# Performance work log

Measured on AMD Instinct MI355X. Metric: run time of the kernel, lower is better.

## Reference

```python
import jax, jax.numpy as jnp
import numpy as np

N_NODES = 100000
N_EDGES = 1600000
D = 128
N_GRAPHS = 8


def setup_inputs() -> dict:
    key = jax.random.key(0)
    ks = jax.random.split(key, 10)
    x = jax.random.normal(ks[0], (N_NODES, D), dtype=jnp.float32)
    src = jax.random.randint(ks[1], (N_EDGES,), 0, N_NODES)
    dst = jax.random.randint(ks[2], (N_EDGES,), 0, N_NODES)
    graph_ids = jnp.sort(jax.random.randint(ks[3], (N_NODES,), 0, N_GRAPHS))
    s = 1.0 / np.sqrt(D)
    W1 = jax.random.normal(ks[4], (D, D), dtype=jnp.float32) * s
    b1 = jnp.zeros((D,), dtype=jnp.float32)
    W2 = jax.random.normal(ks[5], (D, D), dtype=jnp.float32) * s
    b2 = jnp.zeros((D,), dtype=jnp.float32)
    prelu_a = jnp.full((1,), 0.25, dtype=jnp.float32)
    lin_W = jax.random.normal(ks[6], (D, 1), dtype=jnp.float32) * s
    lin_b = jnp.zeros((1,), dtype=jnp.float32)
    return {"x": x, "src": src, "dst": dst, "graph_ids": graph_ids,
            "W1": W1, "b1": b1, "W2": W2, "b2": b2,
            "prelu_a": prelu_a, "lin_W": lin_W, "lin_b": lin_b}


def _gcn_layer(h, src, dst, n_src, n_dst, W, b):
    # GraphConv with symmetric ('both') normalization: D^{-1/2} A D^{-1/2} H W + b
    h = h @ W                                      # [N, D] small GEMM
    m = h[src] * n_src[:, None]                    # [E, D] gather (irregular)
    agg = jax.ops.segment_sum(m, dst, num_segments=N_NODES)  # scatter-add
    return agg * n_dst[:, None] + b


def reference(x, src, dst, graph_ids, W1, b1, W2, b2, prelu_a, lin_W, lin_b):
    ones_e = jnp.ones((src.shape[0],), dtype=x.dtype)
    deg_out = jnp.maximum(jax.ops.segment_sum(ones_e, src, num_segments=N_NODES), 1.0)
    deg_in = jnp.maximum(jax.ops.segment_sum(ones_e, dst, num_segments=N_NODES), 1.0)
    n_src = jax.lax.rsqrt(deg_out)[src]            # per-edge source norm
    n_dst = jax.lax.rsqrt(deg_in)                  # per-node dest norm

    h = _gcn_layer(x, src, dst, n_src, n_dst, W1, b1)
    h = jax.nn.relu(h)
    h = _gcn_layer(h, src, dst, n_src, n_dst, W2, b2)
    h = jax.nn.relu(h)

    # dgl.mean_nodes: per-graph mean over nodes
    sums = jax.ops.segment_sum(h, graph_ids, num_segments=N_GRAPHS)   # [G, D]
    cnt = jax.ops.segment_sum(jnp.ones((N_NODES,), h.dtype), graph_ids,
                              num_segments=N_GRAPHS)
    pooled = sums / jnp.maximum(cnt, 1.0)[:, None]

    # PReLU (single shared slope) -> Linear -> Sigmoid
    pooled = jnp.where(pooled > 0, pooled, prelu_a[0] * pooled)
    out = jax.nn.sigmoid(pooled @ lin_W + lin_b)   # [G, 1]
    return out
```

## Files before the change

kernel.cpp:

```cpp
#include <hip/hip_runtime.h>
#include <hip/hip_bf16.h>

#define NN 100000
#define NE 1600000
#define DD 128
#define NG 8

#define BSH 8
#define KB 391
#define BMASK 255
#define PB 512
#define CHUNK 3125
#define SCAN_N (KB * PB)
#define GHB 98

typedef unsigned short u16;
typedef unsigned char u8;
typedef __attribute__((ext_vector_type(8))) short short8;
typedef __attribute__((ext_vector_type(4))) float f32x4;
typedef __attribute__((ext_vector_type(2))) float f32x2;

static __device__ __forceinline__ u16 f2bf(float f) {
  unsigned u = __float_as_uint(f);
  u += 0x7fffu + ((u >> 16) & 1);
  return (u16)(u >> 16);
}
static __device__ __forceinline__ u8 f2fp8(float f) {
  return (u8)(__builtin_amdgcn_cvt_pk_fp8_f32(f, f, 0, false) & 0xFF);
}

__global__ void conv_xscale(const float* __restrict__ in, const float* __restrict__ rs_out,
                            u8* __restrict__ out, int n8) {
  int i = blockIdx.x * blockDim.x + threadIdx.x;
  if (i >= n8) return;
  float w = rs_out[i >> 4];
  const float4* p = (const float4*)(in + (size_t)i * 8);
  float4 a = p[0], b = p[1];
  int lo = 0, hi = 0;
  lo = __builtin_amdgcn_cvt_pk_fp8_f32(a.x * w, a.y * w, lo, false);
  lo = __builtin_amdgcn_cvt_pk_fp8_f32(a.z * w, a.w * w, lo, true);
  hi = __builtin_amdgcn_cvt_pk_fp8_f32(b.x * w, b.y * w, hi, false);
  hi = __builtin_amdgcn_cvt_pk_fp8_f32(b.z * w, b.w * w, hi, true);
  ((uint2*)out)[i] = make_uint2((unsigned)lo, (unsigned)hi);
}

__global__ __launch_bounds__(256) void p1x(const int* __restrict__ src,
                                           const int* __restrict__ dst,
                                           int* __restrict__ countsS,
                                           int* __restrict__ countsD,
                                           const float* __restrict__ W1,
                                           const float* __restrict__ W2,
                                           u16* __restrict__ Wt1,
                                           u16* __restrict__ Wt2,
                                           const int* __restrict__ gid,
                                           int* __restrict__ cnt_part,
                                           float* __restrict__ pooled) {
  __shared__ int hs[KB], hd[KB];
  __shared__ int h8[NG];
  int t = threadIdx.x, b = blockIdx.x;
  if (b < PB) {
    for (int i = t; i < KB; i += 256) { hs[i] = 0; hd[i] = 0; }
    __syncthreads();
    int e0 = b * CHUNK;
    for (int i = t; i < CHUNK; i += 256) {
      atomicAdd(&hs[src[e0 + i] >> BSH], 1);
      atomicAdd(&hd[dst[e0 + i] >> BSH], 1);
    }
    __syncthreads();
    for (int i = t; i < KB; i += 256) {
      countsS[i * PB + b] = hs[i];
      countsD[i * PB + b] = hd[i];
    }
  } else if (b < PB + 128) {
    int i = (b - PB) * 256 + t;
    if (i < DD * DD) {
      int n = i >> 7, k = i & 127;
      Wt1[i] = f2bf(W1[k * DD + n]);
    } else {
      int i2 = i - DD * DD;
      int n = i2 >> 7, k = i2 & 127;
      Wt2[i2] = f2bf(W2[k * DD + n]);
    }
  } else if (b < PB + 128 + GHB) {
    int blk = b - PB - 128;
    if (t < NG) h8[t] = 0;
    __syncthreads();
    for (int i = blk * 256 + t; i < NN; i += GHB * 256)
      atomicAdd(&h8[gid[i]], 1);
    __syncthreads();
    if (t < NG) cnt_part[blk * NG + t] = h8[t];
  } else {
    for (int i = t; i < NG * DD; i += 256) pooled[i] = 0.f;
  }
}

__global__ __launch_bounds__(256) void scanA(int* __restrict__ countsS,
                                             int* __restrict__ countsD,
                                             int* __restrict__ totS,
                                             int* __restrict__ totD) {
  __shared__ int data[PB];
  __shared__ int part[256];
  int b = blockIdx.x;
  int isS = (b < KB);
  int k = isS ? b : b - KB;
  int* counts = isS ? countsS : countsD;
  int* tot = isS ? totS : totD;
  int t = threadIdx.x;
  int* c = counts + (size_t)k * PB;
  data[t] = c[t];
  data[t + 256] = c[t + 256];
  __syncthreads();
  int a0 = data[2 * t], a1 = data[2 * t + 1];
  int s = a0 + a1;
  part[t] = s;
  __syncthreads();
  for (int off = 1; off < 256; off <<= 1) {
    int v = (t >= off) ? part[t - off] : 0;
    __syncthreads();
    part[t] += v;
    __syncthreads();
  }
  int ex = part[t] - s;
  data[2 * t] = ex;
  data[2 * t + 1] = ex + a0;
  __syncthreads();
  c[t] = data[t];
  c[t + 256] = data[t + 256];
  if (t == 255) tot[k] = part[255];
}

__global__ __launch_bounds__(256) void scanB(const int* __restrict__ totS,
                                             const int* __restrict__ totD,
                                             int* __restrict__ baseS,
                                             int* __restrict__ baseD) {
  __shared__ int data[512];
  __shared__ int part[256];
  const int* tot = blockIdx.x ? totD : totS;
  int* base = blockIdx.x ? baseD : baseS;
  int t = threadIdx.x;
  data[t] = (t < KB) ? tot[t] : 0;
  data[t + 256] = (t + 256 < KB) ? tot[t + 256] : 0;
  __syncthreads();
  int a0 = data[2 * t], a1 = data[2 * t + 1];
  int s = a0 + a1;
  part[t] = s;
  __syncthreads();
  for (int off = 1; off < 256; off <<= 1) {
    int v = (t >= off) ? part[t - off] : 0;
    __syncthreads();
    part[t] += v;
    __syncthreads();
  }
  int ex = part[t] - s;
  int i0 = 2 * t, i1 = 2 * t + 1;
  if (i0 <= KB) base[i0] = ex;
  if (i1 <= KB) base[i1] = ex + a0;
}

__global__ __launch_bounds__(256) void p2_both(const int* __restrict__ src,
                                               const int* __restrict__ dst,
                                               const int* __restrict__ countsS,
                                               const int* __restrict__ countsD,
                                               const int* __restrict__ baseS,
                                               const int* __restrict__ baseD,
                                               u8* __restrict__ recsS,
                                               unsigned* __restrict__ recsD) {
  __shared__ int curS[KB], curD[KB];
  int t = threadIdx.x, blk = blockIdx.x;
  for (int i = t; i < KB; i += 256) {
    curS[i] = countsS[i * PB + blk] + baseS[i];
    curD[i] = countsD[i * PB + blk] + baseD[i];
  }
  __syncthreads();
  int e0 = blk * CHUNK;
  for (int i = t; i < CHUNK; i += 256) {
    int s = src[e0 + i];
    int d = dst[e0 + i];
    int ps = atomicAdd(&curS[s >> BSH], 1);
    recsS[ps] = (u8)(s & BMASK);
    int pd = atomicAdd(&curD[d >> BSH], 1);
    recsD[pd] = (unsigned)s | ((unsigned)(d & BMASK) << 17);
  }
}

__global__ __launch_bounds__(256) void sd_p3(const u8* __restrict__ recsS,
                                             const int* __restrict__ baseS,
                                             float* __restrict__ rs_out,
                                             const unsigned* __restrict__ recsD,
                                             const int* __restrict__ baseD,
                                             int* __restrict__ csr_src,
                                             int* __restrict__ cursor_end,
                                             int* __restrict__ deg_in,
                                             float* __restrict__ rs_in) {
  __shared__ int hist[256];
  __shared__ int part[256];
  int t = threadIdx.x;
  if (blockIdx.x < KB) {
    int k = blockIdx.x;
    int rbeg = baseS[k];
    int rend = baseS[k + 1];
    hist[t] = 0;
    __syncthreads();
    for (int i = rbeg + t; i < rend; i += 256) atomicAdd(&hist[recsS[i]], 1);
    __syncthreads();
    int n = (k << BSH) + t;
    if (n < NN) rs_out[n] = rsqrtf(fmaxf((float)hist[t], 1.f));
  } else {
    int k = blockIdx.x - KB;
    int rbeg = baseD[k];
    int rend = baseD[k + 1];
    hist[t] = 0;
    __syncthreads();
    for (int i = rbeg + t; i < rend; i += 256) atomicAdd(&hist[recsD[i] >> 17], 1);
    __syncthreads();
    int h = hist[t];
    part[t] = h;
    __syncthreads();
    for (int off = 1; off < 256; off <<= 1) {
      int v = (t >= off) ? part[t - off] : 0;
      __syncthreads();
      part[t] += v;
      __syncthreads();
    }
    int run = rbeg + part[t] - h;
    int n = (k << BSH) + t;
    if (n < NN) {
      cursor_end[n] = run + h;
      deg_in[n] = h;
      rs_in[n] = rsqrtf(fmaxf((float)h, 1.f));
    }
    hist[t] = run;
    __syncthreads();
    for (int i = rbeg + t; i < rend; i += 256) {
      unsigned r = recsD[i];
      int pos = atomicAdd(&hist[r >> 17], 1);
      csr_src[pos] = (int)(r & 0x1FFFF);
    }
  }
}

__global__ __launch_bounds__(256) void gather_agg_fp8(
    const uint4* __restrict__ Hv, const int* __restrict__ csr_src,
    const int* __restrict__ cursor_end, const int* __restrict__ deg_in,
    u16* __restrict__ agg) {
  int node = blockIdx.x * 32 + (threadIdx.x >> 3);
  if (node >= NN) return;
  int q = threadIdx.x & 7;
  int end = cursor_end[node];
  int j = end - deg_in[node];
  float acc[16];
#pragma unroll
  for (int i = 0; i < 16; ++i) acc[i] = 0.f;
#define ACCV(v) { f32x2 t_;                                                        \
  t_ = __builtin_amdgcn_cvt_pk_f32_fp8((int)(v).x, false); acc[0] += t_.x;  acc[1] += t_.y;  \
  t_ = __builtin_amdgcn_cvt_pk_f32_fp8((int)(v).x, true);  acc[2] += t_.x;  acc[3] += t_.y;  \
  t_ = __builtin_amdgcn_cvt_pk_f32_fp8((int)(v).y, false); acc[4] += t_.x;  acc[5] += t_.y;  \
  t_ = __builtin_amdgcn_cvt_pk_f32_fp8((int)(v).y, true);  acc[6] += t_.x;  acc[7] += t_.y;  \
  t_ = __builtin_amdgcn_cvt_pk_f32_fp8((int)(v).z, false); acc[8] += t_.x;  acc[9] += t_.y;  \
  t_ = __builtin_amdgcn_cvt_pk_f32_fp8((int)(v).z, true);  acc[10] += t_.x; acc[11] += t_.y; \
  t_ = __builtin_amdgcn_cvt_pk_f32_fp8((int)(v).w, false); acc[12] += t_.x; acc[13] += t_.y; \
  t_ = __builtin_amdgcn_cvt_pk_f32_fp8((int)(v).w, true);  acc[14] += t_.x; acc[15] += t_.y; }
  for (; j + 4 <= end; j += 4) {
    int s0 = csr_src[j + 0];
    int s1 = csr_src[j + 1];
    int s2 = csr_src[j + 2];
    int s3 = csr_src[j + 3];
    uint4 v0 = Hv[(size_t)s0 * 8 + q];
    uint4 v1 = Hv[(size_t)s1 * 8 + q];
    uint4 v2 = Hv[(size_t)s2 * 8 + q];
    uint4 v3 = Hv[(size_t)s3 * 8 + q];
    ACCV(v0) ACCV(v1) ACCV(v2) ACCV(v3)
  }
  for (; j < end; ++j) {
    uint4 v = Hv[(size_t)csr_src[j] * 8 + q];
    ACCV(v)
  }
#undef ACCV
  uint4 o0, o1;
  o0.x = (unsigned)f2bf(acc[0])  | ((unsigned)f2bf(acc[1])  << 16);
  o0.y = (unsigned)f2bf(acc[2])  | ((unsigned)f2bf(acc[3])  << 16);
  o0.z = (unsigned)f2bf(acc[4])  | ((unsigned)f2bf(acc[5])  << 16);
  o0.w = (unsigned)f2bf(acc[6])  | ((unsigned)f2bf(acc[7])  << 16);
  o1.x = (unsigned)f2bf(acc[8])  | ((unsigned)f2bf(acc[9])  << 16);
  o1.y = (unsigned)f2bf(acc[10]) | ((unsigned)f2bf(acc[11]) << 16);
  o1.z = (unsigned)f2bf(acc[12]) | ((unsigned)f2bf(acc[13]) << 16);
  o1.w = (unsigned)f2bf(acc[14]) | ((unsigned)f2bf(acc[15]) << 16);
  u16* op = agg + (size_t)node * DD + q * 16;
  *(uint4*)op = o0;
  *(uint4*)(op + 8) = o1;
}

#define GEMM_PRE                                                              \
  __shared__ uint4 Wl4[2048];                                      \
  int tid = threadIdx.x;                                                      \
  {                                                                           \
    const uint4* Wg4 = (const uint4*)Wt;                                      \
    for (int i = tid; i < 2048; i += 256) {                                   \
      int row = i >> 4, c = i & 15;                                           \
      Wl4[(row << 4) | (c ^ (row & 15))] = Wg4[i];                            \
    }                                                                         \
  }                                                                           \
  int wid = tid >> 6;                                                         \
  int lane = tid & 63;                                                        \
  int l15 = lane & 15;                                                        \
  int kg = lane >> 4;                                                         \
  int rowbase = blockIdx.x * 128 + wid * 32;                                  \
  f32x4 acc[2][8];                                                            \
  short8 a[2][4];                                                             \
  _Pragma("unroll")                                                           \
  for (int t = 0; t < 2; ++t) {                                               \
    int arow = rowbase + t * 16 + l15;                                        \
    bool ok = arow < NN;                                                      \
    const u16* aptr = Ab + (size_t)arow * DD + kg * 8;                        \
    _Pragma("unroll")                                                         \
    for (int kt = 0; kt < 4; ++kt) {                                          \
      a[t][kt] = ok ? *(const short8*)(aptr + kt * 32)                        \
                    : (short8){0, 0, 0, 0, 0, 0, 0, 0};                       \
      acc[0][kt] = (f32x4){0.f, 0.f, 0.f, 0.f};                               \
      acc[0][kt + 4] = (f32x4){0.f, 0.f, 0.f, 0.f};                           \
      acc[1][kt] = (f32x4){0.f, 0.f, 0.f, 0.f};                               \
      acc[1][kt + 4] = (f32x4){0.f, 0.f, 0.f, 0.f};                           \
    }                                                                         \
  }                                                                           \
  __syncthreads();                                                            \
  _Pragma("unroll")                                                           \
  for (int n = 0; n < 8; ++n) {                                               \
    _Pragma("unroll")                                                         \
    for (int kt = 0; kt < 4; ++kt) {                                          \
      short8 b = *(const short8*)(Wl4 + (((n * 16 + l15) << 4) |              \
                                         ((kg + kt * 4) ^ l15)));             \
      acc[0][n] = __builtin_amdgcn_mfma_f32_16x16x32_bf16(a[0][kt], b, acc[0][n], 0, 0, 0); \
      acc[1][n] = __builtin_amdgcn_mfma_f32_16x16x32_bf16(a[1][kt], b, acc[1][n], 0, 0, 0); \
    }                                                                         \
  }

__global__ __launch_bounds__(256) void gemm_mfma_fp8out(
    const u16* __restrict__ Ab, const u16* __restrict__ Wt,
    const float* __restrict__ bias, const float* __restrict__ rs,
    const float* __restrict__ post, u8* __restrict__ Cb) {
  GEMM_PRE
#pragma unroll
  for (int t = 0; t < 2; ++t) {
    int crow0 = rowbase + t * 16 + kg * 4;
#pragma unroll
    for (int j = 0; j < 4; ++j) {
      int r = crow0 + j;
      if (r < NN) {
        float s = rs[r];
        float ps = post[r];
#pragma unroll
        for (int n = 0; n < 8; ++n) {
          float v = fmaxf(acc[t][n][j] * s + bias[n * 16 + l15], 0.f) * ps;
          Cb[(size_t)r * DD + n * 16 + l15] = f2fp8(v);
        }
      }
    }
  }
}

__global__ __launch_bounds__(256) void gemm_mfma_pool(
    const u16* __restrict__ Ab, const u16* __restrict__ Wt,
    const float* __restrict__ bias, const float* __restrict__ rs,
    const int* __restrict__ gid, float* __restrict__ pooled) {
  __shared__ float pl[NG * DD];
  for (int i = threadIdx.x; i < NG * DD; i += 256) pl[i] = 0.f;
  GEMM_PRE
  float pacc[8];
#pragma unroll
  for (int n = 0; n < 8; ++n) pacc[n] = 0.f;
  int curg = -1;
#pragma unroll
  for (int t = 0; t < 2; ++t) {
    int crow0 = rowbase + t * 16 + kg * 4;
#pragma unroll
    for (int j = 0; j < 4; ++j) {
      int r = crow0 + j;
      if (r < NN) {
        int g = gid[r];
        if (g != curg) {
          if (curg >= 0) {
#pragma unroll
            for (int n = 0; n < 8; ++n) {
              atomicAdd(&pl[curg * DD + n * 16 + l15], pacc[n]);
              pacc[n] = 0.f;
            }
          }
          curg = g;
        }
        float s = rs[r];
#pragma unroll
        for (int n = 0; n < 8; ++n)
          pacc[n] += fmaxf(acc[t][n][j] * s + bias[n * 16 + l15], 0.f);
      }
    }
  }
  if (curg >= 0) {
#pragma unroll
    for (int n = 0; n < 8; ++n)
      atomicAdd(&pl[curg * DD + n * 16 + l15], pacc[n]);
  }
  __syncthreads();
  int rlo = blockIdx.x * 128;
  int rhi = rlo + 127;
  if (rhi >= NN) rhi = NN - 1;
  int gmin = gid[rlo];
  int gmax = gid[rhi];
  int span = (gmax - gmin + 1) * DD;
  for (int i = tid; i < span; i += 256) {
    float v = pl[gmin * DD + i];
    if (v != 0.f) atomicAdd(&pooled[gmin * DD + i], v);
  }
}

__global__ __launch_bounds__(128) void final_kernel(const float* __restrict__ pooled,
                                                    const int* __restrict__ cnt_part,
                                                    const float* __restrict__ prelu_a,
                                                    const float* __restrict__ linW,
                                                    const float* __restrict__ linb,
                                                    float* __restrict__ out) {
  int t = threadIdx.x;
  __shared__ float red[2];
  __shared__ int cntl[NG];
  if (t < NG) {
    int s = 0;
    for (int b = 0; b < GHB; ++b) s += cnt_part[b * NG + t];
    cntl[t] = s;
  }
  __syncthreads();
  float w = linW[t];
  float alpha = prelu_a[0];
  float lb = linb[0];
  for (int g = 0; g < NG; ++g) {
    float v = pooled[g * DD + t] / fmaxf((float)cntl[g], 1.f);
    v = v > 0.f ? v : alpha * v;
    float p = v * w;
#pragma unroll
    for (int off = 32; off >= 1; off >>= 1) p += __shfl_down(p, off, 64);
    if ((t & 63) == 0) red[t >> 6] = p;
    __syncthreads();
    if (t == 0) {
      float s = red[0] + red[1] + lb;
      out[g] = 1.f / (1.f + expf(-s));
    }
    __syncthreads();
  }
}

extern "C" void kernel_launch(void* const* d_in, const int* in_sizes, int n_in,
                              void* d_out, int out_size, void* d_ws, size_t ws_size,
                              hipStream_t stream) {
  const float* x   = (const float*)d_in[0];
  const int*   src = (const int*)d_in[1];
  const int*   dst = (const int*)d_in[2];
  const int*   gid = (const int*)d_in[3];
  const float* W1  = (const float*)d_in[4];
  const float* b1  = (const float*)d_in[5];
  const float* W2  = (const float*)d_in[6];
  const float* b2  = (const float*)d_in[7];
  const float* pa  = (const float*)d_in[8];
  const float* lW  = (const float*)d_in[9];
  const float* lb  = (const float*)d_in[10];
  float* out = (float*)d_out;

  char* ws = (char*)d_ws;
  size_t o = 0;
  auto alloc = [&](size_t bytes) {
    size_t r = o;
    o += (bytes + 255) & ~(size_t)255;
    return r;
  };
  int*   deg_in  = (int*)(ws + alloc((size_t)NN * 4));
  float* rs_out  = (float*)(ws + alloc((size_t)NN * 4));
  float* rs_in   = (float*)(ws + alloc((size_t)NN * 4));
  int*   countsS = (int*)(ws + alloc((size_t)SCAN_N * 4));
  int*   countsD = (int*)(ws + alloc((size_t)SCAN_N * 4));
  int*   totS    = (int*)(ws + alloc((size_t)KB * 4));
  int*   totD    = (int*)(ws + alloc((size_t)KB * 4));
  int*   baseS   = (int*)(ws + alloc((size_t)(KB + 1) * 4));
  int*   baseD   = (int*)(ws + alloc((size_t)(KB + 1) * 4));
  int*   cursor_end = (int*)(ws + alloc((size_t)NN * 4));
  u8*    recsS   = (u8*)(ws + alloc((size_t)NE));
  unsigned* recsD = (unsigned*)(ws + alloc((size_t)NE * 4));
  int*   csr_src = (int*)(ws + alloc((size_t)NE * 4));
  u16*   Wt1     = (u16*)(ws + alloc((size_t)DD * DD * 2));
  u16*   Wt2     = (u16*)(ws + alloc((size_t)DD * DD * 2));
  u8*    bufA    = (u8*)(ws + alloc((size_t)NN * DD));
  u8*    bufB    = (u8*)(ws + alloc((size_t)NN * DD));
  u16*   aggbuf  = (u16*)(ws + alloc((size_t)NN * DD * 2));
  float* pooled  = (float*)(ws + alloc((size_t)NG * DD * 4));
  int*   cnt_part = (int*)(ws + alloc((size_t)GHB * NG * 4));

  p1x<<<PB + 128 + GHB + 1, 256, 0, stream>>>(src, dst, countsS, countsD,
                                              W1, W2, Wt1, Wt2, gid, cnt_part, pooled);
  scanA<<<2 * KB, 256, 0, stream>>>(countsS, countsD, totS, totD);
  scanB<<<2, 256, 0, stream>>>(totS, totD, baseS, baseD);
  p2_both<<<PB, 256, 0, stream>>>(src, dst, countsS, countsD, baseS, baseD, recsS, recsD);
  sd_p3<<<2 * KB, 256, 0, stream>>>(recsS, baseS, rs_out,
                                    recsD, baseD, csr_src, cursor_end, deg_in, rs_in);
  conv_xscale<<<(NN * DD / 8 + 255) / 256, 256, 0, stream>>>(x, rs_out, bufA, NN * DD / 8);

  const int gablocks = (NN + 31) / 32;
  const int gmblocks = (NN + 127) / 128;

  gather_agg_fp8<<<gablocks, 256, 0, stream>>>((const uint4*)bufA, csr_src, cursor_end, deg_in, aggbuf);
  gemm_mfma_fp8out<<<gmblocks, 256, 0, stream>>>(aggbuf, Wt1, b1, rs_in, rs_out, bufB);
  gather_agg_fp8<<<gablocks, 256, 0, stream>>>((const uint4*)bufB, csr_src, cursor_end, deg_in, aggbuf);
  gemm_mfma_pool<<<gmblocks, 256, 0, stream>>>(aggbuf, Wt2, b2, rs_in, gid, pooled);
  final_kernel<<<1, 128, 0, stream>>>(pooled, cnt_part, pa, lW, lb, out);
}
```

Measured before the change: 196.7 us.

## Fuse scanB into scatter, fold x fp8 conversion into degree kernel, widen gather

The tiny two-block scanB kernel goes away: every p2x block recomputes the block-total prefix scan in shared memory, and block 0 writes the bases out. The standalone conv_xscale kernel is folded into the source-degree half of sd_p3x, so each block scales and converts its 256 nodes of x to fp8 right after computing rsqrt(deg_out). The gather loop now aligns to 4 and loads csr_src as int4 with 8 gathers in flight. This removes two launches and their serial gaps, at the cost of redundant scan work in every p2x block and a less parallel x-conversion tail.

```diff
diff --git a/kernel.cpp b/kernel.cpp
--- a/kernel.cpp
+++ b/kernel.cpp
@@ -27,21 +27,6 @@
 }
 static __device__ __forceinline__ u8 f2fp8(float f) {
   return (u8)(__builtin_amdgcn_cvt_pk_fp8_f32(f, f, 0, false) & 0xFF);
-}
-
-__global__ void conv_xscale(const float* __restrict__ in, const float* __restrict__ rs_out,
-                            u8* __restrict__ out, int n8) {
-  int i = blockIdx.x * blockDim.x + threadIdx.x;
-  if (i >= n8) return;
-  float w = rs_out[i >> 4];
-  const float4* p = (const float4*)(in + (size_t)i * 8);
-  float4 a = p[0], b = p[1];
-  int lo = 0, hi = 0;
-  lo = __builtin_amdgcn_cvt_pk_fp8_f32(a.x * w, a.y * w, lo, false);
-  lo = __builtin_amdgcn_cvt_pk_fp8_f32(a.z * w, a.w * w, lo, true);
-  hi = __builtin_amdgcn_cvt_pk_fp8_f32(b.x * w, b.y * w, hi, false);
-  hi = __builtin_amdgcn_cvt_pk_fp8_f32(b.z * w, b.w * w, hi, true);
-  ((uint2*)out)[i] = make_uint2((unsigned)lo, (unsigned)hi);
 }
 
 __global__ __launch_bounds__(256) void p1x(const int* __restrict__ src,
@@ -129,47 +114,53 @@
   if (t == 255) tot[k] = part[255];
 }
 
-__global__ __launch_bounds__(256) void scanB(const int* __restrict__ totS,
-                                             const int* __restrict__ totD,
-                                             int* __restrict__ baseS,
-                                             int* __restrict__ baseD) {
+__global__ __launch_bounds__(256) void p2x(const int* __restrict__ src,
+                                           const int* __restrict__ dst,
+                                           const int* __restrict__ countsS,
+                                           const int* __restrict__ countsD,
+                                           const int* __restrict__ totS,
+                                           const int* __restrict__ totD,
+                                           int* __restrict__ baseS,
+                                           int* __restrict__ baseD,
+                                           u8* __restrict__ recsS,
+                                           unsigned* __restrict__ recsD) {
   __shared__ int data[512];
   __shared__ int part[256];
-  const int* tot = blockIdx.x ? totD : totS;
-  int* base = blockIdx.x ? baseD : baseS;
-  int t = threadIdx.x;
-  data[t] = (t < KB) ? tot[t] : 0;
-  data[t + 256] = (t + 256 < KB) ? tot[t + 256] : 0;
-  __syncthreads();
-  int a0 = data[2 * t], a1 = data[2 * t + 1];
-  int s = a0 + a1;
-  part[t] = s;
-  __syncthreads();
-  for (int off = 1; off < 256; off <<= 1) {
-    int v = (t >= off) ? part[t - off] : 0;
-    __syncthreads();
-    part[t] += v;
-    __syncthreads();
-  }
-  int ex = part[t] - s;
-  int i0 = 2 * t, i1 = 2 * t + 1;
-  if (i0 <= KB) base[i0] = ex;
-  if (i1 <= KB) base[i1] = ex + a0;
-}
-
-__global__ __launch_bounds__(256) void p2_both(const int* __restrict__ src,
-                                               const int* __restrict__ dst,
-                                               const int* __restrict__ countsS,
-                                               const int* __restrict__ countsD,
-                                               const int* __restrict__ baseS,
-                                               const int* __restrict__ baseD,
-                                               u8* __restrict__ recsS,
-                                               unsigned* __restrict__ recsD) {
+  __shared__ int bS[KB + 1], bD[KB + 1];
   __shared__ int curS[KB], curD[KB];
   int t = threadIdx.x, blk = blockIdx.x;
+#pragma unroll
+  for (int pass = 0; pass < 2; ++pass) {
+    const int* tot = pass ? totD : totS;
+    int* bb = pass ? bD : bS;
+    data[t] = (t < KB) ? tot[t] : 0;
+    data[t + 256] = (t + 256 < KB) ? tot[t + 256] : 0;
+    __syncthreads();
+    int a0 = data[2 * t], a1 = data[2 * t + 1];
+    int s = a0 + a1;
+    part[t] = s;
+    __syncthreads();
+    for (int off = 1; off < 256; off <<= 1) {
+      int v = (t >= off) ? part[t - off] : 0;
+      __syncthreads();
+      part[t] += v;
+      __syncthreads();
+    }
+    int ex = part[t] - s;
+    int i0 = 2 * t, i1 = 2 * t + 1;
+    if (i0 <= KB) bb[i0] = ex;
+    if (i1 <= KB) bb[i1] = ex + a0;
+    __syncthreads();
+  }
   for (int i = t; i < KB; i += 256) {
-    curS[i] = countsS[i * PB + blk] + baseS[i];
-    curD[i] = countsD[i * PB + blk] + baseD[i];
+    curS[i] = countsS[i * PB + blk] + bS[i];
+    curD[i] = countsD[i * PB + blk] + bD[i];
+  }
+  if (blk == 0) {
+    for (int i = t; i <= KB; i += 256) {
+      baseS[i] = bS[i];
+      baseD[i] = bD[i];
+    }
   }
   __syncthreads();
   int e0 = blk * CHUNK;
@@ -183,17 +174,20 @@
   }
 }
 
-__global__ __launch_bounds__(256) void sd_p3(const u8* __restrict__ recsS,
-                                             const int* __restrict__ baseS,
-                                             float* __restrict__ rs_out,
-                                             const unsigned* __restrict__ recsD,
-                                             const int* __restrict__ baseD,
-                                             int* __restrict__ csr_src,
-                                             int* __restrict__ cursor_end,
-                                             int* __restrict__ deg_in,
-                                             float* __restrict__ rs_in) {
+__global__ __launch_bounds__(256) void sd_p3x(const u8* __restrict__ recsS,
+                                              const int* __restrict__ baseS,
+                                              float* __restrict__ rs_out,
+                                              const float* __restrict__ x,
+                                              u8* __restrict__ bufA,
+                                              const unsigned* __restrict__ recsD,
+                                              const int* __restrict__ baseD,
+                                              int* __restrict__ csr_src,
+                                              int* __restrict__ cursor_end,
+                                              int* __restrict__ deg_in,
+                                              float* __restrict__ rs_in) {
   __shared__ int hist[256];
   __shared__ int part[256];
+  __shared__ float rsl[256];
   int t = threadIdx.x;
   if (blockIdx.x < KB) {
     int k = blockIdx.x;
@@ -203,8 +197,26 @@
     __syncthreads();
     for (int i = rbeg + t; i < rend; i += 256) atomicAdd(&hist[recsS[i]], 1);
     __syncthreads();
-    int n = (k << BSH) + t;
-    if (n < NN) rs_out[n] = rsqrtf(fmaxf((float)hist[t], 1.f));
+    int nbase = k << BSH;
+    int n = nbase + t;
+    float rv = rsqrtf(fmaxf((float)hist[t], 1.f));
+    rsl[t] = rv;
+    if (n < NN) rs_out[n] = rv;
+    __syncthreads();
+    for (int i = t; i < 256 * 16; i += 256) {
+      int row = i >> 4, c = i & 15;
+      int node = nbase + row;
+      if (node >= NN) break;
+      float w = rsl[row];
+      const float4* p = (const float4*)(x + (size_t)node * DD + c * 8);
+      float4 a = p[0], b = p[1];
+      int lo = 0, hi = 0;
+      lo = __builtin_amdgcn_cvt_pk_fp8_f32(a.x * w, a.y * w, lo, false);
+      lo = __builtin_amdgcn_cvt_pk_fp8_f32(a.z * w, a.w * w, lo, true);
+      hi = __builtin_amdgcn_cvt_pk_fp8_f32(b.x * w, b.y * w, hi, false);
+      hi = __builtin_amdgcn_cvt_pk_fp8_f32(b.z * w, b.w * w, hi, true);
+      *(uint2*)(bufA + (size_t)node * DD + c * 8) = make_uint2((unsigned)lo, (unsigned)hi);
+    }
   } else {
     int k = blockIdx.x - KB;
     int rbeg = baseD[k];
@@ -260,16 +272,31 @@
   t_ = __builtin_amdgcn_cvt_pk_f32_fp8((int)(v).z, true);  acc[10] += t_.x; acc[11] += t_.y; \
   t_ = __builtin_amdgcn_cvt_pk_f32_fp8((int)(v).w, false); acc[12] += t_.x; acc[13] += t_.y; \
   t_ = __builtin_amdgcn_cvt_pk_f32_fp8((int)(v).w, true);  acc[14] += t_.x; acc[15] += t_.y; }
-  for (; j + 4 <= end; j += 4) {
-    int s0 = csr_src[j + 0];
-    int s1 = csr_src[j + 1];
-    int s2 = csr_src[j + 2];
-    int s3 = csr_src[j + 3];
-    uint4 v0 = Hv[(size_t)s0 * 8 + q];
-    uint4 v1 = Hv[(size_t)s1 * 8 + q];
-    uint4 v2 = Hv[(size_t)s2 * 8 + q];
-    uint4 v3 = Hv[(size_t)s3 * 8 + q];
+  for (; j < end && (j & 3); ++j) {
+    uint4 v = Hv[(size_t)csr_src[j] * 8 + q];
+    ACCV(v)
+  }
+  for (; j + 8 <= end; j += 8) {
+    int4 sa = *(const int4*)(csr_src + j);
+    int4 sb = *(const int4*)(csr_src + j + 4);
+    uint4 v0 = Hv[(size_t)sa.x * 8 + q];
+    uint4 v1 = Hv[(size_t)sa.y * 8 + q];
+    uint4 v2 = Hv[(size_t)sa.z * 8 + q];
+    uint4 v3 = Hv[(size_t)sa.w * 8 + q];
+    uint4 v4 = Hv[(size_t)sb.x * 8 + q];
+    uint4 v5 = Hv[(size_t)sb.y * 8 + q];
+    uint4 v6 = Hv[(size_t)sb.z * 8 + q];
+    uint4 v7 = Hv[(size_t)sb.w * 8 + q];
+    ACCV(v0) ACCV(v1) ACCV(v2) ACCV(v3) ACCV(v4) ACCV(v5) ACCV(v6) ACCV(v7)
+  }
+  if (j + 4 <= end) {
+    int4 sa = *(const int4*)(csr_src + j);
+    uint4 v0 = Hv[(size_t)sa.x * 8 + q];
+    uint4 v1 = Hv[(size_t)sa.y * 8 + q];
+    uint4 v2 = Hv[(size_t)sa.z * 8 + q];
+    uint4 v3 = Hv[(size_t)sa.w * 8 + q];
     ACCV(v0) ACCV(v1) ACCV(v2) ACCV(v3)
+    j += 4;
   }
   for (; j < end; ++j) {
     uint4 v = Hv[(size_t)csr_src[j] * 8 + q];
@@ -493,11 +520,10 @@
   p1x<<<PB + 128 + GHB + 1, 256, 0, stream>>>(src, dst, countsS, countsD,
                                               W1, W2, Wt1, Wt2, gid, cnt_part, pooled);
   scanA<<<2 * KB, 256, 0, stream>>>(countsS, countsD, totS, totD);
-  scanB<<<2, 256, 0, stream>>>(totS, totD, baseS, baseD);
-  p2_both<<<PB, 256, 0, stream>>>(src, dst, countsS, countsD, baseS, baseD, recsS, recsD);
-  sd_p3<<<2 * KB, 256, 0, stream>>>(recsS, baseS, rs_out,
-                                    recsD, baseD, csr_src, cursor_end, deg_in, rs_in);
-  conv_xscale<<<(NN * DD / 8 + 255) / 256, 256, 0, stream>>>(x, rs_out, bufA, NN * DD / 8);
+  p2x<<<PB, 256, 0, stream>>>(src, dst, countsS, countsD, totS, totD,
+                              baseS, baseD, recsS, recsD);
+  sd_p3x<<<2 * KB, 256, 0, stream>>>(recsS, baseS, rs_out, x, bufA,
+                                     recsD, baseD, csr_src, cursor_end, deg_in, rs_in);
 
   const int gablocks = (NN + 31) / 32;
   const int gmblocks = (NN + 127) / 128;
```

New measurement: 211.1 us. 1.07x slower.
